# Optimization experiments

Hardware: AMD Instinct MI355X
Metric: run time of the kernel (lower is better)

The kernel has to match this reference:

```python
import jax, jax.numpy as jnp
import numpy as np

B, S, D = 8, 2048, 512  # batch, seq_len, dim_val == dim_attn

def setup_inputs() -> dict:
    key = jax.random.key(0)
    kx, kq, kk, kv = jax.random.split(key, 4)
    scale = 1.0 / np.sqrt(D)
    return {
        "x": jax.random.normal(kx, (B, S, D), dtype=jnp.float32),
        "Wq": jax.random.normal(kq, (D, D), dtype=jnp.float32) * scale,  # dim_input -> dim_attn
        "Wk": jax.random.normal(kk, (D, D), dtype=jnp.float32) * scale,
        "Wv": jax.random.normal(kv, (D, D), dtype=jnp.float32) * scale,  # dim_input -> dim_val
    }

def reference(x, Wq, Wk, Wv):
    # bias-free linear projections (nn.Linear stores W as [out,in]; here W is [in,out])
    Q = jnp.einsum("bsd,de->bse", x, Wq)
    K = jnp.einsum("bsd,de->bse", x, Wk)
    V = jnp.einsum("bsd,de->bse", x, Wv)
    # manual scaled dot-product attention: softmax(QK^T / sqrt(d_attn)) V
    scores = jnp.einsum("bqe,bke->bqk", Q, K) / jnp.sqrt(jnp.asarray(Q.shape[-1], Q.dtype))
    a = jax.nn.softmax(scores, axis=-1)
    return jnp.einsum("bqk,bkd->bqd", a, V)
```

## Files before the change

kernel.cpp:

```cpp
#include <hip/hip_runtime.h>


typedef __attribute__((ext_vector_type(8))) short bf16x8;
typedef __attribute__((ext_vector_type(4))) float f32x4;

__device__ __forceinline__ short f2bf(float f) {
  union { float f; unsigned u; } v; v.f = f;
  unsigned r = v.u + 0x7fffu + ((v.u >> 16) & 1u);
  return (short)(r >> 16);
}

__device__ __forceinline__ void async_cp16(const void* g, void* l) {
  __builtin_amdgcn_global_load_lds(
      (const __attribute__((address_space(1))) unsigned int*)g,
      (__attribute__((address_space(3))) unsigned int*)l, 16, 0, 0);
}

__global__ __launch_bounds__(256) void prep_kernel(const float* __restrict__ x,
                                                   const float* __restrict__ Wq,
                                                   const float* __restrict__ Wk,
                                                   const float* __restrict__ Wv,
                                                   short* __restrict__ WT,
                                                   short* __restrict__ xb) {
  if (blockIdx.x < 384) {
    int g = blockIdx.x * 256 + threadIdx.x;
    int w = g >> 15;
    int rem = g & 32767;
    int n = rem & 511;
    int k0 = (rem >> 9) << 3;
    const float* W = (w == 0) ? Wq : ((w == 1) ? Wk : Wv);
    bf16x8 o;
#pragma unroll
    for (int j = 0; j < 8; ++j) o[j] = f2bf(W[(k0 + j) * 512 + n]);
    *(bf16x8*)(WT + w * 262144 + n * 512 + k0) = o;
  } else {
    size_t g = (size_t)(blockIdx.x - 384) * 256 + threadIdx.x;
    size_t off = g * 8;
    f32x4 lo = *(const f32x4*)(x + off);
    f32x4 hi = *(const f32x4*)(x + off + 4);
    bf16x8 o;
    o[0] = f2bf(lo[0]); o[1] = f2bf(lo[1]); o[2] = f2bf(lo[2]); o[3] = f2bf(lo[3]);
    o[4] = f2bf(hi[0]); o[5] = f2bf(hi[1]); o[6] = f2bf(hi[2]); o[7] = f2bf(hi[3]);
    *(bf16x8*)(xb + off) = o;
  }
}

__global__ __launch_bounds__(256, 3) void proj_kernel(const short* __restrict__ xb,
                                                      const short* __restrict__ WT,
                                                      short* __restrict__ QP,
                                                      short* __restrict__ KP,
                                                      short* __restrict__ VP) {
  __shared__ __align__(16) short smem[10240];
  short* Af = smem;
  short* Bf = smem + 4096;
  short* Tb = smem;

  const int tid = threadIdx.x, wv = tid >> 6, ln = tid & 63;
  const int lane_m = ln & 15, lane_q = ln >> 4;
  const int m0 = blockIdx.x * 128, n0 = blockIdx.y * 64;
  const int wm = wv & 1, wn = wv >> 1;

  f32x4 zero4 = {0.f, 0.f, 0.f, 0.f};
  f32x4 acc[3][4][2];
#pragma unroll
  for (int z = 0; z < 3; ++z)
#pragma unroll
    for (int i = 0; i < 4; ++i)
#pragma unroll
      for (int j = 0; j < 2; ++j) acc[z][i][j] = zero4;

#pragma unroll 1
  for (int kk = 0; kk < 16; ++kk) {
    const int k0 = kk * 32;
    __syncthreads();
#pragma unroll
    for (int i = 0; i < 2; ++i) {
      const int mt = wv * 2 + i;
      async_cp16(xb + (size_t)(m0 + mt * 16 + lane_m) * 512 + k0 + lane_q * 8, Af + mt * 512);
    }
#pragma unroll
    for (int z = 0; z < 3; ++z)
      async_cp16(WT + z * 262144 + (size_t)(n0 + wv * 16 + lane_m) * 512 + k0 + lane_q * 8,
                 Bf + z * 2048 + wv * 512);
    __syncthreads();
    bf16x8 a[4];
#pragma unroll
    for (int mi = 0; mi < 4; ++mi) a[mi] = *(bf16x8*)(Af + ((wm * 4 + mi) * 512) + ln * 8);
#pragma unroll
    for (int z = 0; z < 3; ++z) {
      bf16x8 b0 = *(bf16x8*)(Bf + z * 2048 + (wn * 2 + 0) * 512 + ln * 8);
      bf16x8 b1 = *(bf16x8*)(Bf + z * 2048 + (wn * 2 + 1) * 512 + ln * 8);
#pragma unroll
      for (int mi = 0; mi < 4; ++mi) {
        acc[z][mi][0] = __builtin_amdgcn_mfma_f32_16x16x32_bf16(a[mi], b0, acc[z][mi][0], 0, 0, 0);
        acc[z][mi][1] = __builtin_amdgcn_mfma_f32_16x16x32_bf16(a[mi], b1, acc[z][mi][1], 0, 0, 0);
      }
    }
  }

  const int bb = m0 >> 11, tg = (m0 & 2047) >> 6;

#pragma unroll
  for (int z = 0; z < 2; ++z) {
    __syncthreads();
#pragma unroll
    for (int mi = 0; mi < 4; ++mi)
#pragma unroll
      for (int nj = 0; nj < 2; ++nj)
#pragma unroll
        for (int rr = 0; rr < 4; ++rr)
          Tb[(wm * 64 + mi * 16 + lane_q * 4 + rr) * 72 + wn * 32 + nj * 16 + lane_m] =
              f2bf(acc[z][mi][nj][rr]);
    __syncthreads();
    short* Odst = (z == 0) ? QP : KP;
    const int ks0 = n0 >> 5;
#pragma unroll
    for (int p = 0; p < 4; ++p) {
      const int c2 = p * 256 + tid;
      const int ktl = c2 >> 9, wvv = (c2 >> 7) & 3, ksl = (c2 >> 6) & 1;
      const int lq = (c2 >> 4) & 3, lm = c2 & 15;
      const short* src = Tb + (ktl * 64 + wvv * 16 + lm) * 72 + ksl * 32 + lq * 8;
      size_t chunk = (size_t)bb * 131072 + (size_t)(tg + ktl) * 4096 + wvv * 1024 +
                     (ks0 + ksl) * 64 + lq * 16 + lm;
      *(bf16x8*)(Odst + chunk * 8) = *(const bf16x8*)src;
    }
  }
  {
    __syncthreads();
#pragma unroll
    for (int mi = 0; mi < 4; ++mi)
#pragma unroll
      for (int nj = 0; nj < 2; ++nj)
#pragma unroll
        for (int rr = 0; rr < 4; ++rr)
          Tb[(wn * 32 + nj * 16 + lane_m) * 136 + wm * 64 + mi * 16 + lane_q * 4 + rr] =
              f2bf(acc[2][mi][nj][rr]);
    __syncthreads();
    const int wvv2 = n0 >> 7, nt0 = (n0 & 127) >> 4;
#pragma unroll
    for (int p = 0; p < 4; ++p) {
      const int c2 = p * 256 + tid;
      const int ktl = c2 >> 9, ntl = (c2 >> 7) & 3, ks2 = (c2 >> 6) & 1;
      const int lq = (c2 >> 4) & 3, lm = c2 & 15;
      const short* src = Tb + (ntl * 16 + lm) * 136 + ktl * 64 + ks2 * 32 + lq * 8;
      size_t chunk = (size_t)bb * 131072 + (size_t)(tg + ktl) * 4096 + wvv2 * 1024 +
                     (nt0 + ntl) * 128 + ks2 * 64 + lq * 16 + lm;
      *(bf16x8*)(VP + chunk * 8) = *(const bf16x8*)src;
    }
  }
}


#define ISSUE_K(ka0_, ka1_, ka2_, ka3_)                                      \
  asm volatile("global_load_dwordx4 %0, %16, %20\n\t"                        \
               "global_load_dwordx4 %1, %16, %20 offset:1024\n\t"            \
               "global_load_dwordx4 %2, %16, %20 offset:2048\n\t"            \
               "global_load_dwordx4 %3, %16, %20 offset:3072\n\t"            \
               "global_load_dwordx4 %4, %17, %20\n\t"                        \
               "global_load_dwordx4 %5, %17, %20 offset:1024\n\t"            \
               "global_load_dwordx4 %6, %17, %20 offset:2048\n\t"            \
               "global_load_dwordx4 %7, %17, %20 offset:3072\n\t"            \
               "global_load_dwordx4 %8, %18, %20\n\t"                        \
               "global_load_dwordx4 %9, %18, %20 offset:1024\n\t"            \
               "global_load_dwordx4 %10, %18, %20 offset:2048\n\t"           \
               "global_load_dwordx4 %11, %18, %20 offset:3072\n\t"           \
               "global_load_dwordx4 %12, %19, %20\n\t"                       \
               "global_load_dwordx4 %13, %19, %20 offset:1024\n\t"           \
               "global_load_dwordx4 %14, %19, %20 offset:2048\n\t"           \
               "global_load_dwordx4 %15, %19, %20 offset:3072\n\t"           \
               : "=&v"(kfr[0]), "=&v"(kfr[1]), "=&v"(kfr[2]), "=&v"(kfr[3]), \
                 "=&v"(kfr[4]), "=&v"(kfr[5]), "=&v"(kfr[6]), "=&v"(kfr[7]), \
                 "=&v"(kfr[8]), "=&v"(kfr[9]), "=&v"(kfr[10]), "=&v"(kfr[11]), \
                 "=&v"(kfr[12]), "=&v"(kfr[13]), "=&v"(kfr[14]), "=&v"(kfr[15]) \
               : "v"(ka0_), "v"(ka1_), "v"(ka2_), "v"(ka3_), "s"(Kp))

#define ISSUE_V0(va0_, va1_, va2_, va3_)                                     \
  asm volatile("global_load_dwordx4 %0, %8, %12\n\t"                         \
               "global_load_dwordx4 %1, %8, %12 offset:1024\n\t"             \
               "global_load_dwordx4 %2, %9, %12\n\t"                         \
               "global_load_dwordx4 %3, %9, %12 offset:1024\n\t"             \
               "global_load_dwordx4 %4, %10, %12\n\t"                        \
               "global_load_dwordx4 %5, %10, %12 offset:1024\n\t"            \
               "global_load_dwordx4 %6, %11, %12\n\t"                        \
               "global_load_dwordx4 %7, %11, %12 offset:1024\n\t"            \
               : "=&v"(v0[0]), "=&v"(v0[1]), "=&v"(v0[2]), "=&v"(v0[3]),     \
                 "=&v"(v0[4]), "=&v"(v0[5]), "=&v"(v0[6]), "=&v"(v0[7])      \
               : "v"(va0_), "v"(va1_), "v"(va2_), "v"(va3_), "s"(VTp))

#define ISSUE_V1(va0_, va1_, va2_, va3_)                                     \
  asm volatile("global_load_dwordx4 %0, %8, %12\n\t"                         \
               "global_load_dwordx4 %1, %8, %12 offset:1024\n\t"             \
               "global_load_dwordx4 %2, %9, %12\n\t"                         \
               "global_load_dwordx4 %3, %9, %12 offset:1024\n\t"             \
               "global_load_dwordx4 %4, %10, %12\n\t"                        \
               "global_load_dwordx4 %5, %10, %12 offset:1024\n\t"            \
               "global_load_dwordx4 %6, %11, %12\n\t"                        \
               "global_load_dwordx4 %7, %11, %12 offset:1024\n\t"            \
               : "=&v"(v1[0]), "=&v"(v1[1]), "=&v"(v1[2]), "=&v"(v1[3]),     \
                 "=&v"(v1[4]), "=&v"(v1[5]), "=&v"(v1[6]), "=&v"(v1[7])      \
               : "v"(va0_), "v"(va1_), "v"(va2_), "v"(va3_), "s"(VTp))

#define WAITK()                                                              \
  asm volatile("s_waitcnt vmcnt(8)"                                          \
               : "+v"(kfr[0]), "+v"(kfr[1]), "+v"(kfr[2]), "+v"(kfr[3]),     \
                 "+v"(kfr[4]), "+v"(kfr[5]), "+v"(kfr[6]), "+v"(kfr[7]),     \
                 "+v"(kfr[8]), "+v"(kfr[9]), "+v"(kfr[10]), "+v"(kfr[11]),   \
                 "+v"(kfr[12]), "+v"(kfr[13]), "+v"(kfr[14]), "+v"(kfr[15]))

#define WAITV()                                                              \
  asm volatile("s_waitcnt vmcnt(0)"                                          \
               : "+v"(v0[0]), "+v"(v0[1]), "+v"(v0[2]), "+v"(v0[3]),         \
                 "+v"(v0[4]), "+v"(v0[5]), "+v"(v0[6]), "+v"(v0[7]),         \
                 "+v"(v1[0]), "+v"(v1[1]), "+v"(v1[2]), "+v"(v1[3]),         \
                 "+v"(v1[4]), "+v"(v1[5]), "+v"(v1[6]), "+v"(v1[7]))

#define DRAIN_K()                                                            \
  asm volatile("s_waitcnt vmcnt(0)"                                          \
               : "+v"(kfr[0]), "+v"(kfr[1]), "+v"(kfr[2]), "+v"(kfr[3]),     \
                 "+v"(kfr[4]), "+v"(kfr[5]), "+v"(kfr[6]), "+v"(kfr[7]),     \
                 "+v"(kfr[8]), "+v"(kfr[9]), "+v"(kfr[10]), "+v"(kfr[11]),   \
                 "+v"(kfr[12]), "+v"(kfr[13]), "+v"(kfr[14]), "+v"(kfr[15]))

#define PV_STEP(kc_, VARR)                                                     \
  {                                                                            \
    bf16x8 pa0 = *(bf16x8*)(pfb + (((kc_) * 4 + 0) * 64 + effr) * 8);          \
    bf16x8 pa1 = *(bf16x8*)(pfb + (((kc_) * 4 + 1) * 64 + effr) * 8);          \
    bf16x8 pa2 = *(bf16x8*)(pfb + (((kc_) * 4 + 2) * 64 + effr) * 8);          \
    bf16x8 pa3 = *(bf16x8*)(pfb + (((kc_) * 4 + 3) * 64 + effr) * 8);          \
    _Pragma("unroll")                                                          \
    for (int ntl = 0; ntl < 4; ++ntl) {                                        \
      bf16x8 bv = VARR[ntl * 2 + ((kc_)&1)];                                   \
      O[0][ntl] = __builtin_amdgcn_mfma_f32_16x16x32_bf16(pa0, bv, O[0][ntl], 0, 0, 0); \
      O[1][ntl] = __builtin_amdgcn_mfma_f32_16x16x32_bf16(pa1, bv, O[1][ntl], 0, 0, 0); \
      O[2][ntl] = __builtin_amdgcn_mfma_f32_16x16x32_bf16(pa2, bv, O[2][ntl], 0, 0, 0); \
      O[3][ntl] = __builtin_amdgcn_mfma_f32_16x16x32_bf16(pa3, bv, O[3][ntl], 0, 0, 0); \
    }                                                                          \
  }

__global__ __launch_bounds__(512, 2) void flash_kernel(const short* __restrict__ Q,
                                                       const short* __restrict__ K,
                                                       const short* __restrict__ VT,
                                                       float* __restrict__ out) {
  __shared__ __align__(16) short qf[32768];
  __shared__ __align__(16) short pf[16384];
  __shared__ float l_red[8][64];

  const int tid = threadIdx.x, w = tid >> 6, ln = tid & 63;
  const int lane_m = ln & 15, lane_q = ln >> 4;
  const int b = blockIdx.x & 7, qt = blockIdx.x >> 3;
  const int m0 = qt * 64;
  const short* Qp = Q + (size_t)b * 1048576;
  const short* Kp = K + (size_t)b * 1048576;
  const short* VTp = VT + (size_t)b * 1048576;
  const float sc2 = 0.044194173824159216f * 1.4426950408889634f;

#pragma unroll
  for (int r = 0; r < 8; ++r) {
    const int region = w * 8 + r;
    const int mi = region & 3, ks = region >> 2;
    const short* src = Qp + ((size_t)(qt * 4096 + mi * 1024 + ks * 64) + ln) * 8;
    *(bf16x8*)(qf + (region * 64 + ln) * 8) = *(const bf16x8*)src;
  }

  f32x4 zero4 = {0.f, 0.f, 0.f, 0.f};
  f32x4 O[4][4];
#pragma unroll
  for (int mi = 0; mi < 4; ++mi)
#pragma unroll
    for (int ntl = 0; ntl < 4; ++ntl) O[mi][ntl] = zero4;

  float lp[4][4] = {{0.f, 0.f, 0.f, 0.f}, {0.f, 0.f, 0.f, 0.f},
                    {0.f, 0.f, 0.f, 0.f}, {0.f, 0.f, 0.f, 0.f}};

  const unsigned kvb = (unsigned)((w >> 2) * 65536 + (w & 3) * 16384 + ln * 16);
  const unsigned vvb = (unsigned)((w >> 1) * 16384 + (w & 1) * 8192 + ln * 16);
  const int quad = ((w & 1) << 1) | (lane_m >> 3);
  const int jj = lane_m & 7;
  const int effr = ln ^ (ln >> 4);
  const int preg = (w >> 1) << 2;

  __syncthreads();

  bf16x8 kfr[16], v0[8], v1[8];
  ISSUE_K(kvb, kvb + 4096u, kvb + 8192u, kvb + 12288u);

#pragma unroll 1
  for (int kt = 0; kt < 16; ++kt) {
    const unsigned va0 = vvb + (unsigned)(kt * 131072);
    const unsigned va1 = va0 + 2048u, va2 = va0 + 4096u, va3 = va0 + 6144u;
    ISSUE_V0(va0, va1, va2, va3);
    WAITK();
    f32x4 s[4] = {zero4, zero4, zero4, zero4};
#pragma unroll
    for (int ks = 0; ks < 12; ++ks) {
#pragma unroll
      for (int mi = 0; mi < 4; ++mi) {
        bf16x8 a = *(bf16x8*)(qf + ((ks * 4 + mi) * 64 + ln) * 8);
        s[mi] = __builtin_amdgcn_mfma_f32_16x16x32_bf16(a, kfr[ks], s[mi], 0, 0, 0);
      }
    }
    ISSUE_V1(va0 + 65536u, va1 + 65536u, va2 + 65536u, va3 + 65536u);
#pragma unroll
    for (int ks = 12; ks < 16; ++ks) {
#pragma unroll
      for (int mi = 0; mi < 4; ++mi) {
        bf16x8 a = *(bf16x8*)(qf + ((ks * 4 + mi) * 64 + ln) * 8);
        s[mi] = __builtin_amdgcn_mfma_f32_16x16x32_bf16(a, kfr[ks], s[mi], 0, 0, 0);
      }
    }
    short* pfb = pf + (kt & 1) * 8192;
#pragma unroll
    for (int mi = 0; mi < 4; ++mi)
#pragma unroll
      for (int rr = 0; rr < 4; ++rr) {
        const int m = lane_q * 4 + rr;
        const int eff = (m ^ quad) + quad * 16;
        float p = exp2f(s[mi][rr] * sc2 - 12.0f);
        lp[mi][rr] += p;
        pfb[((preg + mi) * 64 + eff) * 8 + jj] = f2bf(p);
      }
    __syncthreads();

    WAITV();
    PV_STEP(0, v0);
    {
      const unsigned ka0 = kvb + (unsigned)(((kt + 1) & 15) * 131072);
      ISSUE_K(ka0, ka0 + 4096u, ka0 + 8192u, ka0 + 12288u);
    }
    PV_STEP(1, v0);
    PV_STEP(2, v1);
    PV_STEP(3, v1);
  }
  DRAIN_K();

#pragma unroll
  for (int mi = 0; mi < 4; ++mi)
#pragma unroll
    for (int rr = 0; rr < 4; ++rr) {
      float v = lp[mi][rr];
      v += __shfl_xor(v, 1);
      v += __shfl_xor(v, 2);
      v += __shfl_xor(v, 4);
      v += __shfl_xor(v, 8);
      lp[mi][rr] = v;
    }
  if (lane_m == 0) {
#pragma unroll
    for (int mi = 0; mi < 4; ++mi)
#pragma unroll
      for (int rr = 0; rr < 4; ++rr)
        l_red[w][mi * 16 + lane_q * 4 + rr] = lp[mi][rr];
  }
  __syncthreads();

  float linv[4][4];
#pragma unroll
  for (int mi = 0; mi < 4; ++mi)
#pragma unroll
    for (int rr = 0; rr < 4; ++rr) {
      const int row = mi * 16 + lane_q * 4 + rr;
      float l = 0.f;
#pragma unroll
      for (int ww = 0; ww < 8; ++ww) l += l_red[ww][row];
      linv[mi][rr] = 1.f / l;
    }
#pragma unroll
  for (int mi = 0; mi < 4; ++mi)
#pragma unroll
    for (int ntl = 0; ntl < 4; ++ntl)
#pragma unroll
      for (int rr = 0; rr < 4; ++rr) {
        size_t row = (size_t)b * 2048 + m0 + mi * 16 + lane_q * 4 + rr;
        out[row * 512 + w * 64 + ntl * 16 + lane_m] = O[mi][ntl][rr] * linv[mi][rr];
      }
}

extern "C" void kernel_launch(void* const* d_in, const int* in_sizes, int n_in,
                              void* d_out, int out_size, void* d_ws, size_t ws_size,
                              hipStream_t stream) {
  const float* x  = (const float*)d_in[0];
  const float* Wq = (const float*)d_in[1];
  const float* Wk = (const float*)d_in[2];
  const float* Wv = (const float*)d_in[3];
  float* out = (float*)d_out;
  char* ws = (char*)d_ws;
  short* WT = (short*)ws;
  short* QP = (short*)(ws + 1572864);
  short* KP = (short*)(ws + 1572864 + 16777216);
  short* VP = (short*)(ws + 1572864 + 2 * 16777216);
  short* xb = (short*)(ws + 1572864 + 3 * 16777216);

  prep_kernel<<<dim3(384 + 4096), dim3(256), 0, stream>>>(x, Wq, Wk, Wv, WT, xb);
  proj_kernel<<<dim3(128, 8), dim3(256), 0, stream>>>(xb, WT, QP, KP, VP);
  flash_kernel<<<dim3(256), dim3(512), 0, stream>>>(QP, KP, VP, out);
}
```

Before: 210.7 us.

## Double key tile per iteration and rotate four register buffers for K/V prefetch

The flash attention loop now handles 256 keys per iteration (8 iterations instead of 16), with each wave computing two 16-key score columns. K and V fragments share four rotating 8-register buffers: each quarter of S consumes a buffer and immediately refills it with the matching V slice, and each PV quarter refills it with the next K slice, with fine-grained vmcnt waits in between. The aim is to overlap global loads with MFMA work more continuously and to halve the per-iteration barrier and loop overhead. In exchange the P buffer in LDS doubles, which raises LDS use and register pressure under the 512-thread, 2-block launch bounds.

```diff
diff --git a/kernel.cpp b/kernel.cpp
--- a/kernel.cpp
+++ b/kernel.cpp
@@ -151,98 +151,68 @@
 }
 
 
-#define ISSUE_K(ka0_, ka1_, ka2_, ka3_)                                      \
-  asm volatile("global_load_dwordx4 %0, %16, %20\n\t"                        \
-               "global_load_dwordx4 %1, %16, %20 offset:1024\n\t"            \
-               "global_load_dwordx4 %2, %16, %20 offset:2048\n\t"            \
-               "global_load_dwordx4 %3, %16, %20 offset:3072\n\t"            \
-               "global_load_dwordx4 %4, %17, %20\n\t"                        \
-               "global_load_dwordx4 %5, %17, %20 offset:1024\n\t"            \
-               "global_load_dwordx4 %6, %17, %20 offset:2048\n\t"            \
-               "global_load_dwordx4 %7, %17, %20 offset:3072\n\t"            \
-               "global_load_dwordx4 %8, %18, %20\n\t"                        \
-               "global_load_dwordx4 %9, %18, %20 offset:1024\n\t"            \
-               "global_load_dwordx4 %10, %18, %20 offset:2048\n\t"           \
-               "global_load_dwordx4 %11, %18, %20 offset:3072\n\t"           \
-               "global_load_dwordx4 %12, %19, %20\n\t"                       \
-               "global_load_dwordx4 %13, %19, %20 offset:1024\n\t"           \
-               "global_load_dwordx4 %14, %19, %20 offset:2048\n\t"           \
-               "global_load_dwordx4 %15, %19, %20 offset:3072\n\t"           \
-               : "=&v"(kfr[0]), "=&v"(kfr[1]), "=&v"(kfr[2]), "=&v"(kfr[3]), \
-                 "=&v"(kfr[4]), "=&v"(kfr[5]), "=&v"(kfr[6]), "=&v"(kfr[7]), \
-                 "=&v"(kfr[8]), "=&v"(kfr[9]), "=&v"(kfr[10]), "=&v"(kfr[11]), \
-                 "=&v"(kfr[12]), "=&v"(kfr[13]), "=&v"(kfr[14]), "=&v"(kfr[15]) \
-               : "v"(ka0_), "v"(ka1_), "v"(ka2_), "v"(ka3_), "s"(Kp))
-
-#define ISSUE_V0(va0_, va1_, va2_, va3_)                                     \
-  asm volatile("global_load_dwordx4 %0, %8, %12\n\t"                         \
-               "global_load_dwordx4 %1, %8, %12 offset:1024\n\t"             \
-               "global_load_dwordx4 %2, %9, %12\n\t"                         \
-               "global_load_dwordx4 %3, %9, %12 offset:1024\n\t"             \
-               "global_load_dwordx4 %4, %10, %12\n\t"                        \
-               "global_load_dwordx4 %5, %10, %12 offset:1024\n\t"            \
-               "global_load_dwordx4 %6, %11, %12\n\t"                        \
-               "global_load_dwordx4 %7, %11, %12 offset:1024\n\t"            \
-               : "=&v"(v0[0]), "=&v"(v0[1]), "=&v"(v0[2]), "=&v"(v0[3]),     \
-                 "=&v"(v0[4]), "=&v"(v0[5]), "=&v"(v0[6]), "=&v"(v0[7])      \
-               : "v"(va0_), "v"(va1_), "v"(va2_), "v"(va3_), "s"(VTp))
-
-#define ISSUE_V1(va0_, va1_, va2_, va3_)                                     \
-  asm volatile("global_load_dwordx4 %0, %8, %12\n\t"                         \
-               "global_load_dwordx4 %1, %8, %12 offset:1024\n\t"             \
-               "global_load_dwordx4 %2, %9, %12\n\t"                         \
-               "global_load_dwordx4 %3, %9, %12 offset:1024\n\t"             \
-               "global_load_dwordx4 %4, %10, %12\n\t"                        \
-               "global_load_dwordx4 %5, %10, %12 offset:1024\n\t"            \
-               "global_load_dwordx4 %6, %11, %12\n\t"                        \
-               "global_load_dwordx4 %7, %11, %12 offset:1024\n\t"            \
-               : "=&v"(v1[0]), "=&v"(v1[1]), "=&v"(v1[2]), "=&v"(v1[3]),     \
-                 "=&v"(v1[4]), "=&v"(v1[5]), "=&v"(v1[6]), "=&v"(v1[7])      \
-               : "v"(va0_), "v"(va1_), "v"(va2_), "v"(va3_), "s"(VTp))
-
-#define WAITK()                                                              \
-  asm volatile("s_waitcnt vmcnt(8)"                                          \
-               : "+v"(kfr[0]), "+v"(kfr[1]), "+v"(kfr[2]), "+v"(kfr[3]),     \
-                 "+v"(kfr[4]), "+v"(kfr[5]), "+v"(kfr[6]), "+v"(kfr[7]),     \
-                 "+v"(kfr[8]), "+v"(kfr[9]), "+v"(kfr[10]), "+v"(kfr[11]),   \
-                 "+v"(kfr[12]), "+v"(kfr[13]), "+v"(kfr[14]), "+v"(kfr[15]))
-
-#define WAITV()                                                              \
-  asm volatile("s_waitcnt vmcnt(0)"                                          \
-               : "+v"(v0[0]), "+v"(v0[1]), "+v"(v0[2]), "+v"(v0[3]),         \
-                 "+v"(v0[4]), "+v"(v0[5]), "+v"(v0[6]), "+v"(v0[7]),         \
-                 "+v"(v1[0]), "+v"(v1[1]), "+v"(v1[2]), "+v"(v1[3]),         \
-                 "+v"(v1[4]), "+v"(v1[5]), "+v"(v1[6]), "+v"(v1[7]))
-
-#define DRAIN_K()                                                            \
-  asm volatile("s_waitcnt vmcnt(0)"                                          \
-               : "+v"(kfr[0]), "+v"(kfr[1]), "+v"(kfr[2]), "+v"(kfr[3]),     \
-                 "+v"(kfr[4]), "+v"(kfr[5]), "+v"(kfr[6]), "+v"(kfr[7]),     \
-                 "+v"(kfr[8]), "+v"(kfr[9]), "+v"(kfr[10]), "+v"(kfr[11]),   \
-                 "+v"(kfr[12]), "+v"(kfr[13]), "+v"(kfr[14]), "+v"(kfr[15]))
-
-#define PV_STEP(kc_, VARR)                                                     \
-  {                                                                            \
-    bf16x8 pa0 = *(bf16x8*)(pfb + (((kc_) * 4 + 0) * 64 + effr) * 8);          \
-    bf16x8 pa1 = *(bf16x8*)(pfb + (((kc_) * 4 + 1) * 64 + effr) * 8);          \
-    bf16x8 pa2 = *(bf16x8*)(pfb + (((kc_) * 4 + 2) * 64 + effr) * 8);          \
-    bf16x8 pa3 = *(bf16x8*)(pfb + (((kc_) * 4 + 3) * 64 + effr) * 8);          \
-    _Pragma("unroll")                                                          \
-    for (int ntl = 0; ntl < 4; ++ntl) {                                        \
-      bf16x8 bv = VARR[ntl * 2 + ((kc_)&1)];                                   \
-      O[0][ntl] = __builtin_amdgcn_mfma_f32_16x16x32_bf16(pa0, bv, O[0][ntl], 0, 0, 0); \
-      O[1][ntl] = __builtin_amdgcn_mfma_f32_16x16x32_bf16(pa1, bv, O[1][ntl], 0, 0, 0); \
-      O[2][ntl] = __builtin_amdgcn_mfma_f32_16x16x32_bf16(pa2, bv, O[2][ntl], 0, 0, 0); \
-      O[3][ntl] = __builtin_amdgcn_mfma_f32_16x16x32_bf16(pa3, bv, O[3][ntl], 0, 0, 0); \
-    }                                                                          \
-  }
+#define ISSUE8(R, a0_, a1_, B)                                               \
+  asm volatile("global_load_dwordx4 %0, %8, %10\n\t"                         \
+               "global_load_dwordx4 %1, %8, %10 offset:1024\n\t"             \
+               "global_load_dwordx4 %2, %8, %10 offset:2048\n\t"             \
+               "global_load_dwordx4 %3, %8, %10 offset:3072\n\t"             \
+               "global_load_dwordx4 %4, %9, %10\n\t"                         \
+               "global_load_dwordx4 %5, %9, %10 offset:1024\n\t"             \
+               "global_load_dwordx4 %6, %9, %10 offset:2048\n\t"             \
+               "global_load_dwordx4 %7, %9, %10 offset:3072\n\t"             \
+               : "=&v"(R[0]), "=&v"(R[1]), "=&v"(R[2]), "=&v"(R[3]),         \
+                 "=&v"(R[4]), "=&v"(R[5]), "=&v"(R[6]), "=&v"(R[7])          \
+               : "v"(a0_), "v"(a1_), "s"(B))
+
+#define WAIT8(R, N)                                                          \
+  asm volatile("s_waitcnt vmcnt(" #N ")"                                     \
+               : "+v"(R[0]), "+v"(R[1]), "+v"(R[2]), "+v"(R[3]),             \
+                 "+v"(R[4]), "+v"(R[5]), "+v"(R[6]), "+v"(R[7]))
+
+#define MFMA(A, B, C) __builtin_amdgcn_mfma_f32_16x16x32_bf16(A, B, C, 0, 0, 0)
+
+#define S_QUARTER(X, ksq)                                                    \
+  WAIT8(X, 24);                                                              \
+  _Pragma("unroll")                                                          \
+  for (int l = 0; l < 4; ++l) {                                              \
+    _Pragma("unroll")                                                        \
+    for (int mi = 0; mi < 4; ++mi) {                                         \
+      bf16x8 a = *(bf16x8*)(qf + ((((ksq)*4 + l) * 4 + mi) * 64 + ln) * 8);  \
+      s[mi][0] = MFMA(a, X[l], s[mi][0]);                                    \
+      s[mi][1] = MFMA(a, X[4 + l], s[mi][1]);                                \
+    }                                                                        \
+  }
+
+#define PV_QUARTER(X, vq)                                                    \
+  WAIT8(X, 24);                                                              \
+  _Pragma("unroll")                                                          \
+  for (int ks2 = 0; ks2 < 2; ++ks2) {                                        \
+    bf16x8 pa[4];                                                            \
+    _Pragma("unroll")                                                        \
+    for (int mi = 0; mi < 4; ++mi)                                           \
+      pa[mi] = *(bf16x8*)(pfb + ((((vq)*2 + ks2) * 4 + mi) * 64 + effr) * 8);\
+    _Pragma("unroll")                                                        \
+    for (int ntl = 0; ntl < 4; ++ntl) {                                      \
+      _Pragma("unroll")                                                      \
+      for (int mi = 0; mi < 4; ++mi)                                         \
+        O[mi][ntl] = MFMA(pa[mi], X[ntl * 2 + ks2], O[mi][ntl]);             \
+    }                                                                        \
+  }
+
+#define ISSUE_KQ(X, kt_, ksq)                                                \
+  { const unsigned a0 = kb0 + (unsigned)(((kt_) & 7) * 262144) + (ksq)*4096u;\
+    ISSUE8(X, a0, a0 + 16384u, Kp); }
+
+#define ISSUE_VQ(X, kt_, vq)                                                 \
+  { const unsigned a0 = vb0 + (unsigned)((kt_) * 262144) + (vq)*65536u;      \
+    ISSUE8(X, a0, a0 + 4096u, VTp); }
 
 __global__ __launch_bounds__(512, 2) void flash_kernel(const short* __restrict__ Q,
                                                        const short* __restrict__ K,
                                                        const short* __restrict__ VT,
                                                        float* __restrict__ out) {
   __shared__ __align__(16) short qf[32768];
-  __shared__ __align__(16) short pf[16384];
+  __shared__ __align__(16) short pf[32768];
   __shared__ float l_red[8][64];
 
   const int tid = threadIdx.x, w = tid >> 6, ln = tid & 63;
@@ -272,66 +242,58 @@
   float lp[4][4] = {{0.f, 0.f, 0.f, 0.f}, {0.f, 0.f, 0.f, 0.f},
                     {0.f, 0.f, 0.f, 0.f}, {0.f, 0.f, 0.f, 0.f}};
 
-  const unsigned kvb = (unsigned)((w >> 2) * 65536 + (w & 3) * 16384 + ln * 16);
-  const unsigned vvb = (unsigned)((w >> 1) * 16384 + (w & 1) * 8192 + ln * 16);
-  const int quad = ((w & 1) << 1) | (lane_m >> 3);
+  const unsigned kb0 = (unsigned)((w >> 1) * 65536 + (w & 1) * 32768 + ln * 16);
+  const unsigned vb0 = (unsigned)((w >> 1) * 16384 + (w & 1) * 8192 + ln * 16);
   const int jj = lane_m & 7;
   const int effr = ln ^ (ln >> 4);
-  const int preg = (w >> 1) << 2;
 
   __syncthreads();
 
-  bf16x8 kfr[16], v0[8], v1[8];
-  ISSUE_K(kvb, kvb + 4096u, kvb + 8192u, kvb + 12288u);
+  bf16x8 bA[8], bB[8], bC[8], bD[8];
+  ISSUE_KQ(bA, 0, 0);
+  ISSUE_KQ(bB, 0, 1);
+  ISSUE_KQ(bC, 0, 2);
+  ISSUE_KQ(bD, 0, 3);
 
 #pragma unroll 1
-  for (int kt = 0; kt < 16; ++kt) {
-    const unsigned va0 = vvb + (unsigned)(kt * 131072);
-    const unsigned va1 = va0 + 2048u, va2 = va0 + 4096u, va3 = va0 + 6144u;
-    ISSUE_V0(va0, va1, va2, va3);
-    WAITK();
-    f32x4 s[4] = {zero4, zero4, zero4, zero4};
-#pragma unroll
-    for (int ks = 0; ks < 12; ++ks) {
-#pragma unroll
-      for (int mi = 0; mi < 4; ++mi) {
-        bf16x8 a = *(bf16x8*)(qf + ((ks * 4 + mi) * 64 + ln) * 8);
-        s[mi] = __builtin_amdgcn_mfma_f32_16x16x32_bf16(a, kfr[ks], s[mi], 0, 0, 0);
+  for (int kt = 0; kt < 8; ++kt) {
+    f32x4 s[4][2];
+#pragma unroll
+    for (int mi = 0; mi < 4; ++mi) { s[mi][0] = zero4; s[mi][1] = zero4; }
+
+    S_QUARTER(bA, 0); ISSUE_VQ(bA, kt, 0);
+    S_QUARTER(bB, 1); ISSUE_VQ(bB, kt, 1);
+    S_QUARTER(bC, 2); ISSUE_VQ(bC, kt, 2);
+    S_QUARTER(bD, 3); ISSUE_VQ(bD, kt, 3);
+
+    short* pfb = pf + (kt & 1) * 16384;
+#pragma unroll
+    for (int mi = 0; mi < 4; ++mi)
+#pragma unroll
+      for (int kj = 0; kj < 2; ++kj) {
+        const int quad = (kj << 1) | (lane_m >> 3);
+#pragma unroll
+        for (int rr = 0; rr < 4; ++rr) {
+          const int m = lane_q * 4 + rr;
+          const int eff = (m ^ quad) + quad * 16;
+          float p = exp2f(s[mi][kj][rr] * sc2 - 12.0f);
+          lp[mi][rr] += p;
+          pfb[((w * 4 + mi) * 64 + eff) * 8 + jj] = f2bf(p);
+        }
       }
-    }
-    ISSUE_V1(va0 + 65536u, va1 + 65536u, va2 + 65536u, va3 + 65536u);
-#pragma unroll
-    for (int ks = 12; ks < 16; ++ks) {
-#pragma unroll
-      for (int mi = 0; mi < 4; ++mi) {
-        bf16x8 a = *(bf16x8*)(qf + ((ks * 4 + mi) * 64 + ln) * 8);
-        s[mi] = __builtin_amdgcn_mfma_f32_16x16x32_bf16(a, kfr[ks], s[mi], 0, 0, 0);
-      }
-    }
-    short* pfb = pf + (kt & 1) * 8192;
-#pragma unroll
-    for (int mi = 0; mi < 4; ++mi)
-#pragma unroll
-      for (int rr = 0; rr < 4; ++rr) {
-        const int m = lane_q * 4 + rr;
-        const int eff = (m ^ quad) + quad * 16;
-        float p = exp2f(s[mi][rr] * sc2 - 12.0f);
-        lp[mi][rr] += p;
-        pfb[((preg + mi) * 64 + eff) * 8 + jj] = f2bf(p);
-      }
-    __syncthreads();
-
-    WAITV();
-    PV_STEP(0, v0);
-    {
-      const unsigned ka0 = kvb + (unsigned)(((kt + 1) & 15) * 131072);
-      ISSUE_K(ka0, ka0 + 4096u, ka0 + 8192u, ka0 + 12288u);
-    }
-    PV_STEP(1, v0);
-    PV_STEP(2, v1);
-    PV_STEP(3, v1);
-  }
-  DRAIN_K();
+    asm volatile("s_waitcnt lgkmcnt(0)" ::: "memory");
+    __builtin_amdgcn_s_barrier();
+    asm volatile("" ::: "memory");
+
+    PV_QUARTER(bA, 0); ISSUE_KQ(bA, kt + 1, 0);
+    PV_QUARTER(bB, 1); ISSUE_KQ(bB, kt + 1, 1);
+    PV_QUARTER(bC, 2); ISSUE_KQ(bC, kt + 1, 2);
+    PV_QUARTER(bD, 3); ISSUE_KQ(bD, kt + 1, 3);
+  }
+  WAIT8(bA, 0);
+  WAIT8(bB, 0);
+  WAIT8(bC, 0);
+  WAIT8(bD, 0);
 
 #pragma unroll
   for (int mi = 0; mi < 4; ++mi)
```

Result: slower. 243.7 us (+15.7%).
